# Optimization experiments

Hardware: AMD Instinct MI355X
Metric: run time of the kernel (lower is better)

Reference implementation:

```python
import jax, jax.numpy as jnp
import numpy as np

B, C, L = 16, 512, 8192
K = 7  # kernel_size, symmetric padding K//2 = 3


def setup_inputs() -> dict:
    key = jax.random.key(0)
    k1, k2, k3 = jax.random.split(key, 3)
    x = jax.random.normal(k1, (B, C, L), dtype=jnp.float32)
    mask = jax.random.randint(k2, (B, 1, L), 0, 2).astype(bool)
    # Conv1d(2 -> 1, kernel 7, no bias): weight shape (out=1, in=2, k=7)
    conv_w = jax.random.normal(k3, (1, 2, K), dtype=jnp.float32) * (1.0 / np.sqrt(2 * K))
    return {"x": x, "mask": mask, "conv_w": conv_w}


def reference(x, mask, conv_w):
    # Channel-wise max and mean pooling -> (B, 1, L) each
    max_c = jnp.max(x, axis=1, keepdims=True)
    avg_c = jnp.mean(x, axis=1, keepdims=True)
    # NOTE: in the original torch code, every masked_fill_ call uses the
    # out-of-place masked_fill and its return value is discarded, so the mask
    # has NO effect on the computation. We replicate that faithfully: `mask`
    # is accepted but unused.
    feats = jnp.concatenate([max_c, avg_c], axis=1)  # (B, 2, L)
    logits = jax.lax.conv_general_dilated(
        feats, conv_w,
        window_strides=(1,),
        padding=[(K // 2, K // 2)],
        dimension_numbers=("NCH", "OIH", "NCH"),
    )  # (B, 1, L)
    attn = jax.nn.sigmoid(logits)
    return attn * x  # (B, C, L)
```

## Files before the change

### kernel.cpp

```cpp
#include <hip/hip_runtime.h>
#include <math.h>

#define NB 16
#define NC 512
#define NL 8192
#define KW 7
#define NF4 (NL / 4)
#define SLABS 16
#define SCH (NC / SLABS)

__global__ __launch_bounds__(1024) void k1_pool(
    const float* __restrict__ x, float* __restrict__ part) {
    const int blk = blockIdx.x;
    const int b   = blk >> 4;
    const int s   = blk & (SLABS - 1);
    const int tid = threadIdx.x;

    const float* px = x + (size_t)(b * NC + s * SCH) * NL;

    float4 v0 = *(const float4*)(px + 4 * tid);
    float4 v1 = *(const float4*)(px + 4 * (tid + 1024));
    float4 mx0 = v0, sm0 = v0, mx1 = v1, sm1 = v1;

#pragma unroll 4
    for (int c = 1; c < SCH; ++c) {
        const float* pr = px + (size_t)c * NL;
        float4 a = *(const float4*)(pr + 4 * tid);
        float4 bq = *(const float4*)(pr + 4 * (tid + 1024));
        mx0.x = fmaxf(mx0.x, a.x);  sm0.x += a.x;
        mx0.y = fmaxf(mx0.y, a.y);  sm0.y += a.y;
        mx0.z = fmaxf(mx0.z, a.z);  sm0.z += a.z;
        mx0.w = fmaxf(mx0.w, a.w);  sm0.w += a.w;
        mx1.x = fmaxf(mx1.x, bq.x); sm1.x += bq.x;
        mx1.y = fmaxf(mx1.y, bq.y); sm1.y += bq.y;
        mx1.z = fmaxf(mx1.z, bq.z); sm1.z += bq.z;
        mx1.w = fmaxf(mx1.w, bq.w); sm1.w += bq.w;
    }

    float* pm = part + ((size_t)blk * 2 + 0) * NL;
    float* ps = part + ((size_t)blk * 2 + 1) * NL;
    *(float4*)(pm + 4 * tid)          = mx0;
    *(float4*)(pm + 4 * (tid + 1024)) = mx1;
    *(float4*)(ps + 4 * tid)          = sm0;
    *(float4*)(ps + 4 * (tid + 1024)) = sm1;
}

#define K2OUT 250
__global__ __launch_bounds__(256) void k2_conv(
    const float* __restrict__ part, const float* __restrict__ w,
    float* __restrict__ attn) {
    __shared__ float pm[256], pa[256], wl[2 * KW];
    const int nt   = (NL + K2OUT - 1) / K2OUT;
    const int b    = blockIdx.x / nt;
    const int t    = blockIdx.x - b * nt;
    const int base = t * K2OUT;
    const int tid  = threadIdx.x;
    if (tid < 2 * KW) wl[tid] = w[tid];

    const int pc = base - 3 + tid;
    if (pc >= 0 && pc < NL) {
        float m = -INFINITY, sm = 0.0f;
#pragma unroll
        for (int s = 0; s < SLABS; ++s) {
            m  = fmaxf(m, part[(((size_t)b * SLABS + s) * 2 + 0) * NL + pc]);
            sm += part[(((size_t)b * SLABS + s) * 2 + 1) * NL + pc];
        }
        pm[tid] = m;
        pa[tid] = sm * (1.0f / (float)NC);
    } else {
        pm[tid] = 0.0f;
        pa[tid] = 0.0f;
    }
    __syncthreads();

    const int l = base + tid;
    if (tid < K2OUT && l < NL) {
        float logit = 0.0f;
#pragma unroll
        for (int k = 0; k < KW; ++k) {
            logit = fmaf(pm[tid + k], wl[k],      logit);
            logit = fmaf(pa[tid + k], wl[KW + k], logit);
        }
        attn[(size_t)b * NL + l] = 1.0f / (1.0f + expf(-logit));
    }
}

__global__ __launch_bounds__(256) void k3_apply(
    const float* __restrict__ x, const float* __restrict__ attn,
    float* __restrict__ out) {
    const size_t total  = (size_t)NB * NC * NF4;
    const size_t stride = (size_t)gridDim.x * 256;
    for (size_t i = (size_t)blockIdx.x * 256 + threadIdx.x; i < total; i += stride) {
        const int col4 = (int)(i & (NF4 - 1));
        const int b    = (int)(i >> 20);
        float4 xv = *(const float4*)(x + 4 * i);
        float4 at = *(const float4*)(attn + ((size_t)b << 13) + 4 * (size_t)col4);
        float4 o;
        o.x = at.x * xv.x;
        o.y = at.y * xv.y;
        o.z = at.z * xv.z;
        o.w = at.w * xv.w;
        *(float4*)(out + 4 * i) = o;
    }
}

extern "C" void kernel_launch(void* const* d_in, const int* in_sizes, int n_in,
                              void* d_out, int out_size, void* d_ws, size_t ws_size,
                              hipStream_t stream) {
    const float* x = (const float*)d_in[0];
    const float* w = (const float*)d_in[2];
    float* out = (float*)d_out;

    float* part = (float*)d_ws;
    float* attn = part + (size_t)NB * SLABS * 2 * NL;

    k1_pool<<<NB * SLABS, 1024, 0, stream>>>(x, part);
    k2_conv<<<NB * ((NL + K2OUT - 1) / K2OUT), 256, 0, stream>>>(part, w, attn);
    k3_apply<<<2048, 256, 0, stream>>>(x, attn, out);
}
```

Before: 161.6 us.

## Restructure apply kernel to reuse pool slab order, nontemporal stores, hoisted attn

The apply kernel now uses the same slab-per-block decomposition as the pooling kernel. It walks each slab's channels in reverse so the rows k1 touched last, which may still sit in the large last-level cache, are reread first. The attention vector is loaded once per thread and held in registers, and output writes use nontemporal stores to avoid polluting the cache. The trade-off is only 256 blocks of 1024 threads, which gives lower parallelism and latency hiding than the earlier grid-stride launch.

```diff
diff --git a/kernel.cpp b/kernel.cpp
--- a/kernel.cpp
+++ b/kernel.cpp
@@ -5,28 +5,27 @@
 #define NC 512
 #define NL 8192
 #define KW 7
-#define NF4 (NL / 4)
 #define SLABS 16
 #define SCH (NC / SLABS)
+
+typedef float vf4 __attribute__((ext_vector_type(4)));
 
 __global__ __launch_bounds__(1024) void k1_pool(
     const float* __restrict__ x, float* __restrict__ part) {
     const int blk = blockIdx.x;
-    const int b   = blk >> 4;
-    const int s   = blk & (SLABS - 1);
     const int tid = threadIdx.x;
 
-    const float* px = x + (size_t)(b * NC + s * SCH) * NL;
+    const float* px = x + (size_t)blk * SCH * NL;
 
-    float4 v0 = *(const float4*)(px + 4 * tid);
-    float4 v1 = *(const float4*)(px + 4 * (tid + 1024));
-    float4 mx0 = v0, sm0 = v0, mx1 = v1, sm1 = v1;
+    vf4 v0 = *(const vf4*)(px + 4 * tid);
+    vf4 v1 = *(const vf4*)(px + 4 * (tid + 1024));
+    vf4 mx0 = v0, sm0 = v0, mx1 = v1, sm1 = v1;
 
 #pragma unroll 4
     for (int c = 1; c < SCH; ++c) {
         const float* pr = px + (size_t)c * NL;
-        float4 a = *(const float4*)(pr + 4 * tid);
-        float4 bq = *(const float4*)(pr + 4 * (tid + 1024));
+        vf4 a = *(const vf4*)(pr + 4 * tid);
+        vf4 bq = *(const vf4*)(pr + 4 * (tid + 1024));
         mx0.x = fmaxf(mx0.x, a.x);  sm0.x += a.x;
         mx0.y = fmaxf(mx0.y, a.y);  sm0.y += a.y;
         mx0.z = fmaxf(mx0.z, a.z);  sm0.z += a.z;
@@ -39,10 +38,10 @@
 
     float* pm = part + ((size_t)blk * 2 + 0) * NL;
     float* ps = part + ((size_t)blk * 2 + 1) * NL;
-    *(float4*)(pm + 4 * tid)          = mx0;
-    *(float4*)(pm + 4 * (tid + 1024)) = mx1;
-    *(float4*)(ps + 4 * tid)          = sm0;
-    *(float4*)(ps + 4 * (tid + 1024)) = sm1;
+    *(vf4*)(pm + 4 * tid)          = mx0;
+    *(vf4*)(pm + 4 * (tid + 1024)) = mx1;
+    *(vf4*)(ps + 4 * tid)          = sm0;
+    *(vf4*)(ps + 4 * (tid + 1024)) = sm1;
 }
 
 #define K2OUT 250
@@ -85,22 +84,33 @@
     }
 }
 
-__global__ __launch_bounds__(256) void k3_apply(
+__global__ __launch_bounds__(1024) void k3_apply(
     const float* __restrict__ x, const float* __restrict__ attn,
     float* __restrict__ out) {
-    const size_t total  = (size_t)NB * NC * NF4;
-    const size_t stride = (size_t)gridDim.x * 256;
-    for (size_t i = (size_t)blockIdx.x * 256 + threadIdx.x; i < total; i += stride) {
-        const int col4 = (int)(i & (NF4 - 1));
-        const int b    = (int)(i >> 20);
-        float4 xv = *(const float4*)(x + 4 * i);
-        float4 at = *(const float4*)(attn + ((size_t)b << 13) + 4 * (size_t)col4);
-        float4 o;
-        o.x = at.x * xv.x;
-        o.y = at.y * xv.y;
-        o.z = at.z * xv.z;
-        o.w = at.w * xv.w;
-        *(float4*)(out + 4 * i) = o;
+    const int blk = blockIdx.x;
+    const int b   = blk >> 4;
+    const int tid = threadIdx.x;
+
+    const size_t base = (size_t)blk * SCH * NL;
+    const float* px = x + base;
+    float*       po = out + base;
+
+    const vf4 at0 = *(const vf4*)(attn + (size_t)b * NL + 4 * tid);
+    const vf4 at1 = *(const vf4*)(attn + (size_t)b * NL + 4 * (tid + 1024));
+
+#pragma unroll 4
+    for (int c = SCH - 1; c >= 0; --c) {
+        const float* pr = px + (size_t)c * NL;
+        float*       pw = po + (size_t)c * NL;
+        vf4 a  = *(const vf4*)(pr + 4 * tid);
+        vf4 bq = *(const vf4*)(pr + 4 * (tid + 1024));
+        vf4 o0, o1;
+        o0.x = at0.x * a.x;  o0.y = at0.y * a.y;
+        o0.z = at0.z * a.z;  o0.w = at0.w * a.w;
+        o1.x = at1.x * bq.x; o1.y = at1.y * bq.y;
+        o1.z = at1.z * bq.z; o1.w = at1.w * bq.w;
+        __builtin_nontemporal_store(o0, (vf4*)(pw + 4 * tid));
+        __builtin_nontemporal_store(o1, (vf4*)(pw + 4 * (tid + 1024)));
     }
 }
 
@@ -116,5 +126,5 @@
 
     k1_pool<<<NB * SLABS, 1024, 0, stream>>>(x, part);
     k2_conv<<<NB * ((NL + K2OUT - 1) / K2OUT), 256, 0, stream>>>(part, w, attn);
-    k3_apply<<<2048, 256, 0, stream>>>(x, attn, out);
+    k3_apply<<<NB * SLABS, 1024, 0, stream>>>(x, attn, out);
 }
```

After: 144.0 us. -10.9%, faster.

## Process batches in chunks so x stays cache-resident between pool and apply passes

Applied to the files above, without the earlier changes.

Runs the pool, conv and apply kernels per chunk of 8 batches, so the second read of x in the apply pass can hit in the large last-level cache instead of going to HBM. The pool kernel moves to 256-thread blocks with 64 slabs of 8 channels each, and the apply kernel is restructured to the same slab layout with attention held in registers and nontemporal stores. In exchange there are more kernel launches, and the conv kernel now reduces 64 partials per column instead of 16.

```diff
diff --git a/kernel.cpp b/kernel.cpp
--- a/kernel.cpp
+++ b/kernel.cpp
@@ -5,54 +5,59 @@
 #define NC 512
 #define NL 8192
 #define KW 7
+
+#define CHUNKB 8
+#define SLABS 64
+#define SCH (NC / SLABS)
 #define NF4 (NL / 4)
-#define SLABS 16
-#define SCH (NC / SLABS)
+#define FPT (NF4 / 256)
 
-__global__ __launch_bounds__(1024) void k1_pool(
-    const float* __restrict__ x, float* __restrict__ part) {
+typedef float vf4 __attribute__((ext_vector_type(4)));
+
+__global__ __launch_bounds__(256) void k1_pool(
+    const float* __restrict__ x, float* __restrict__ part, int b0) {
     const int blk = blockIdx.x;
-    const int b   = blk >> 4;
+    const int b   = b0 + (blk >> 6);
     const int s   = blk & (SLABS - 1);
     const int tid = threadIdx.x;
 
-    const float* px = x + (size_t)(b * NC + s * SCH) * NL;
+    const float* px = x + ((size_t)b * NC + (size_t)s * SCH) * NL;
 
-    float4 v0 = *(const float4*)(px + 4 * tid);
-    float4 v1 = *(const float4*)(px + 4 * (tid + 1024));
-    float4 mx0 = v0, sm0 = v0, mx1 = v1, sm1 = v1;
-
-#pragma unroll 4
-    for (int c = 1; c < SCH; ++c) {
-        const float* pr = px + (size_t)c * NL;
-        float4 a = *(const float4*)(pr + 4 * tid);
-        float4 bq = *(const float4*)(pr + 4 * (tid + 1024));
-        mx0.x = fmaxf(mx0.x, a.x);  sm0.x += a.x;
-        mx0.y = fmaxf(mx0.y, a.y);  sm0.y += a.y;
-        mx0.z = fmaxf(mx0.z, a.z);  sm0.z += a.z;
-        mx0.w = fmaxf(mx0.w, a.w);  sm0.w += a.w;
-        mx1.x = fmaxf(mx1.x, bq.x); sm1.x += bq.x;
-        mx1.y = fmaxf(mx1.y, bq.y); sm1.y += bq.y;
-        mx1.z = fmaxf(mx1.z, bq.z); sm1.z += bq.z;
-        mx1.w = fmaxf(mx1.w, bq.w); sm1.w += bq.w;
+    vf4 mx[FPT], sm[FPT];
+#pragma unroll
+    for (int i = 0; i < FPT; ++i) {
+        vf4 v = *(const vf4*)(px + 4 * (tid + 256 * i));
+        mx[i] = v; sm[i] = v;
     }
-
-    float* pm = part + ((size_t)blk * 2 + 0) * NL;
-    float* ps = part + ((size_t)blk * 2 + 1) * NL;
-    *(float4*)(pm + 4 * tid)          = mx0;
-    *(float4*)(pm + 4 * (tid + 1024)) = mx1;
-    *(float4*)(ps + 4 * tid)          = sm0;
-    *(float4*)(ps + 4 * (tid + 1024)) = sm1;
+#pragma unroll 2
+    for (int r = 1; r < SCH; ++r) {
+        const float* pr = px + (size_t)r * NL;
+#pragma unroll
+        for (int i = 0; i < FPT; ++i) {
+            vf4 v = *(const vf4*)(pr + 4 * (tid + 256 * i));
+            mx[i].x = fmaxf(mx[i].x, v.x); sm[i].x += v.x;
+            mx[i].y = fmaxf(mx[i].y, v.y); sm[i].y += v.y;
+            mx[i].z = fmaxf(mx[i].z, v.z); sm[i].z += v.z;
+            mx[i].w = fmaxf(mx[i].w, v.w); sm[i].w += v.w;
+        }
+    }
+    float* pm = part + (((size_t)b * SLABS + s) * 2 + 0) * NL;
+    float* ps = part + (((size_t)b * SLABS + s) * 2 + 1) * NL;
+#pragma unroll
+    for (int i = 0; i < FPT; ++i) {
+        *(vf4*)(pm + 4 * (tid + 256 * i)) = mx[i];
+        *(vf4*)(ps + 4 * (tid + 256 * i)) = sm[i];
+    }
 }
 
 #define K2OUT 250
+#define K2NT ((NL + K2OUT - 1) / K2OUT)
 __global__ __launch_bounds__(256) void k2_conv(
     const float* __restrict__ part, const float* __restrict__ w,
-    float* __restrict__ attn) {
+    float* __restrict__ attn, int b0) {
     __shared__ float pm[256], pa[256], wl[2 * KW];
-    const int nt   = (NL + K2OUT - 1) / K2OUT;
-    const int b    = blockIdx.x / nt;
-    const int t    = blockIdx.x - b * nt;
+    const int b    = b0 + blockIdx.x / K2NT;
+    const int t    = blockIdx.x % K2NT;
     const int base = t * K2OUT;
     const int tid  = threadIdx.x;
     if (tid < 2 * KW) wl[tid] = w[tid];
@@ -60,7 +65,7 @@
     const int pc = base - 3 + tid;
     if (pc >= 0 && pc < NL) {
         float m = -INFINITY, sm = 0.0f;
-#pragma unroll
+#pragma unroll 8
         for (int s = 0; s < SLABS; ++s) {
             m  = fmaxf(m, part[(((size_t)b * SLABS + s) * 2 + 0) * NL + pc]);
             sm += part[(((size_t)b * SLABS + s) * 2 + 1) * NL + pc];
@@ -87,20 +92,35 @@
 
 __global__ __launch_bounds__(256) void k3_apply(
     const float* __restrict__ x, const float* __restrict__ attn,
-    float* __restrict__ out) {
-    const size_t total  = (size_t)NB * NC * NF4;
-    const size_t stride = (size_t)gridDim.x * 256;
-    for (size_t i = (size_t)blockIdx.x * 256 + threadIdx.x; i < total; i += stride) {
-        const int col4 = (int)(i & (NF4 - 1));
-        const int b    = (int)(i >> 20);
-        float4 xv = *(const float4*)(x + 4 * i);
-        float4 at = *(const float4*)(attn + ((size_t)b << 13) + 4 * (size_t)col4);
-        float4 o;
-        o.x = at.x * xv.x;
-        o.y = at.y * xv.y;
-        o.z = at.z * xv.z;
-        o.w = at.w * xv.w;
-        *(float4*)(out + 4 * i) = o;
+    float* __restrict__ out, int b0) {
+    const int blk = blockIdx.x;
+    const int b   = b0 + (blk >> 6);
+    const int s   = blk & (SLABS - 1);
+    const int tid = threadIdx.x;
+
+    const size_t base = ((size_t)b * NC + (size_t)s * SCH) * NL;
+    const float* px = x + base;
+    float*       po = out + base;
+
+    vf4 at[FPT];
+#pragma unroll
+    for (int i = 0; i < FPT; ++i)
+        at[i] = *(const vf4*)(attn + (size_t)b * NL + 4 * (tid + 256 * i));
+
+#pragma unroll 2
+    for (int r = 0; r < SCH; ++r) {
+        const float* pr = px + (size_t)r * NL;
+        float*       pw = po + (size_t)r * NL;
+#pragma unroll
+        for (int i = 0; i < FPT; ++i) {
+            vf4 v = *(const vf4*)(pr + 4 * (tid + 256 * i));
+            vf4 o;
+            o.x = at[i].x * v.x;
+            o.y = at[i].y * v.y;
+            o.z = at[i].z * v.z;
+            o.w = at[i].w * v.w;
+            __builtin_nontemporal_store(o, (vf4*)(pw + 4 * (tid + 256 * i)));
+        }
     }
 }
 
@@ -114,7 +134,10 @@
     float* part = (float*)d_ws;
     float* attn = part + (size_t)NB * SLABS * 2 * NL;
 
-    k1_pool<<<NB * SLABS, 1024, 0, stream>>>(x, part);
-    k2_conv<<<NB * ((NL + K2OUT - 1) / K2OUT), 256, 0, stream>>>(part, w, attn);
-    k3_apply<<<2048, 256, 0, stream>>>(x, attn, out);
+    for (int chunk = 0; chunk < NB / CHUNKB; ++chunk) {
+        const int b0 = chunk * CHUNKB;
+        k1_pool<<<CHUNKB * SLABS, 256, 0, stream>>>(x, part, b0);
+        k2_conv<<<CHUNKB * K2NT, 256, 0, stream>>>(part, w, attn, b0);
+        k3_apply<<<CHUNKB * SLABS, 256, 0, stream>>>(x, attn, out, b0);
+    }
 }
```

Result: slower. 169.3 us (+4.8%).
